# Optimization experiments

Measured on AMD Instinct MI355X. Metric: run time of the kernel, lower is better.

The kernel has to match this reference:

```python
import jax, jax.numpy as jnp
import numpy as np

EPS = 1e-5
ALPHA = 0.7
N_HEADS = 20
N_KV_HEADS = 5
HEAD_DIM = 128


def bitlinear(x, w):
    # absmean ternary quantization per output row: w_t = sign(w)*(|w| > alpha*absmean)
    absw = jnp.abs(w)
    absmean = jnp.mean(absw, axis=1, keepdims=True)            # [out, 1]
    tern = jnp.sign(w) * (absw > ALPHA * absmean).astype(w.dtype)
    # (X @ pos^T - X @ neg^T) * scale == (X @ tern^T) * scale
    return jnp.einsum('...i,oi->...o', x, tern) * absmean[:, 0]


def rmsnorm(x, g):
    var = jnp.mean(jnp.square(x), axis=-1, keepdims=True)
    return x * jax.lax.rsqrt(var + EPS) * g


def rotate_half(x):
    x1, x2 = jnp.split(x, 2, axis=-1)
    return jnp.concatenate([-x2, x1], axis=-1)


def setup_inputs() -> dict:
    key = jax.random.key(0)
    ks = jax.random.split(key, 12)
    h, inter = 2560, 6912
    b, s = 1, 2048
    wscale = 1.0 / np.sqrt(h)
    return {
        'x': jax.random.normal(ks[0], (b, s, h), jnp.float32),
        'cos': jax.random.uniform(ks[1], (1, 1, s, HEAD_DIM), jnp.float32),
        'sin': jax.random.uniform(ks[2], (1, 1, s, HEAD_DIM), jnp.float32),
        'q_w': jax.random.normal(ks[3], (h, h), jnp.float32) * wscale,
        'k_w': jax.random.normal(ks[4], (N_KV_HEADS * HEAD_DIM, h), jnp.float32) * wscale,
        'v_w': jax.random.normal(ks[5], (N_KV_HEADS * HEAD_DIM, h), jnp.float32) * wscale,
        'o_w': jax.random.normal(ks[6], (h, h), jnp.float32) * wscale,
        'gate_w': jax.random.normal(ks[7], (inter, h), jnp.float32) * wscale,
        'up_w': jax.random.normal(ks[8], (inter, h), jnp.float32) * wscale,
        'down_w': jax.random.normal(ks[9], (h, inter), jnp.float32) / np.sqrt(inter),
        'ln1_w': jnp.ones((h,), jnp.float32),
        'ln2_w': jnp.ones((h,), jnp.float32),
    }


def reference(x, cos, sin, q_w, k_w, v_w, o_w, gate_w, up_w, down_w, ln1_w, ln2_w):
    b, s, hdim = x.shape
    residual = x
    h = rmsnorm(x, ln1_w)

    q = bitlinear(h, q_w).reshape(b, s, N_HEADS, HEAD_DIM).transpose(0, 2, 1, 3)
    k = bitlinear(h, k_w).reshape(b, s, N_KV_HEADS, HEAD_DIM).transpose(0, 2, 1, 3)
    v = bitlinear(h, v_w).reshape(b, s, N_KV_HEADS, HEAD_DIM).transpose(0, 2, 1, 3)

    # RoPE
    q = q * cos + rotate_half(q) * sin
    k = k * cos + rotate_half(k) * sin

    # GQA: repeat_interleave kv heads
    n_rep = N_HEADS // N_KV_HEADS
    k = jnp.repeat(k, n_rep, axis=1)
    v = jnp.repeat(v, n_rep, axis=1)

    scale = 1.0 / np.sqrt(HEAD_DIM)
    attn = jnp.einsum('bhqd,bhkd->bhqk', q, k) * scale
    attn = jax.nn.softmax(attn, axis=-1)
    o = jnp.einsum('bhqk,bhkd->bhqd', attn, v)
    o = o.transpose(0, 2, 1, 3).reshape(b, s, hdim)

    x = residual + bitlinear(o, o_w)

    residual = x
    h = rmsnorm(x, ln2_w)
    gate = jnp.square(jax.nn.relu(bitlinear(h, gate_w)))  # relu^2
    x = residual + bitlinear(gate * bitlinear(h, up_w), down_w)
    return x
```

## Files before the change

kernel.cpp:

```cpp
#include <hip/hip_runtime.h>
#include <hip/hip_bf16.h>

typedef unsigned short u16;
typedef short bf16x8 __attribute__((ext_vector_type(8)));
typedef float f32x4 __attribute__((ext_vector_type(4)));
typedef float f32x16 __attribute__((ext_vector_type(16)));
typedef float f4 __attribute__((ext_vector_type(4)));
typedef unsigned short u16x4 __attribute__((ext_vector_type(4)));

__device__ __forceinline__ u16 f2b(float f) {
    union { __hip_bfloat16 h; u16 u; } cv;
    cv.h = __float2bfloat16(f);
    return cv.u;
}
__device__ __forceinline__ float b2f(u16 u) {
    union { u16 u; __hip_bfloat16 h; } cv;
    cv.u = u;
    return __bfloat162float(cv.h);
}

__device__ __forceinline__ void g2l16(const void* g, void* l) {
    __builtin_amdgcn_global_load_lds(
        (const __attribute__((address_space(1))) unsigned int*)g,
        (__attribute__((address_space(3))) unsigned int*)l, 16, 0, 0);
}

template <int NV4, int NS>
__global__ __launch_bounds__(256) void quant_kernel(const float* __restrict__ W,
                                                    u16* __restrict__ T,
                                                    float* __restrict__ scales, int K) {
    const int row = blockIdx.x, tid = threadIdx.x;
    const float* wr = W + (size_t)row * K;
    f4 v[NV4];
    float vs[NS];
    float s = 0.f;
#pragma unroll
    for (int j = 0; j < NV4; ++j) {
        v[j] = ((const f4*)wr)[tid + j * 256];
#pragma unroll
        for (int e = 0; e < 4; ++e) s += fabsf(v[j][e]);
    }
#pragma unroll
    for (int j = 0; j < NS; ++j) { vs[j] = wr[NV4 * 1024 + j * 256 + tid]; s += fabsf(vs[j]); }
#pragma unroll
    for (int d = 1; d < 64; d <<= 1) s += __shfl_xor(s, d);
    __shared__ float red[4];
    if ((tid & 63) == 0) red[tid >> 6] = s;
    __syncthreads();
    const float absmean = (red[0] + red[1] + red[2] + red[3]) / (float)K;
    const float thr = 0.7f * absmean;
    u16* tr = T + (size_t)row * K;
#pragma unroll
    for (int j = 0; j < NV4; ++j) {
        u16x4 o;
#pragma unroll
        for (int e = 0; e < 4; ++e) {
            const float w = v[j][e];
            o[e] = (fabsf(w) > thr) ? ((w > 0.f) ? (u16)0x3F80 : (u16)0xBF80) : (u16)0;
        }
        ((u16x4*)tr)[tid + j * 256] = o;
    }
#pragma unroll
    for (int j = 0; j < NS; ++j) {
        const float w = vs[j];
        tr[NV4 * 1024 + j * 256 + tid] = (fabsf(w) > thr) ? ((w > 0.f) ? (u16)0x3F80 : (u16)0xBF80) : (u16)0;
    }
    if (tid == 0) scales[row] = absmean;
}

__global__ __launch_bounds__(256) void rmsnorm_kernel(const float* __restrict__ x,
                                                      const float* __restrict__ g,
                                                      u16* __restrict__ o) {
    const int row = blockIdx.x, tid = threadIdx.x;
    const float* xr = x + (size_t)row * 2560;
    f4 v[2];
    float vs[2];
    float s = 0.f;
#pragma unroll
    for (int j = 0; j < 2; ++j) {
        v[j] = ((const f4*)xr)[tid + j * 256];
#pragma unroll
        for (int e = 0; e < 4; ++e) s += v[j][e] * v[j][e];
    }
#pragma unroll
    for (int j = 0; j < 2; ++j) { vs[j] = xr[2048 + j * 256 + tid]; s += vs[j] * vs[j]; }
#pragma unroll
    for (int d = 1; d < 64; d <<= 1) s += __shfl_xor(s, d);
    __shared__ float red[4];
    if ((tid & 63) == 0) red[tid >> 6] = s;
    __syncthreads();
    const float total = red[0] + red[1] + red[2] + red[3];
    const float rs = rsqrtf(total * (1.f / 2560.f) + 1e-5f);
    u16* orow = o + (size_t)row * 2560;
#pragma unroll
    for (int j = 0; j < 2; ++j) {
        const f4 gv = ((const f4*)g)[tid + j * 256];
        u16x4 ov;
#pragma unroll
        for (int e = 0; e < 4; ++e) ov[e] = f2b(v[j][e] * rs * gv[e]);
        ((u16x4*)orow)[tid + j * 256] = ov;
    }
#pragma unroll
    for (int j = 0; j < 2; ++j)
        orow[2048 + j * 256 + tid] = f2b(vs[j] * rs * g[2048 + j * 256 + tid]);
}

template <int MODE>
__global__ __launch_bounds__(512, 4) void gemm_bt(const u16* __restrict__ A,
                                                  const u16* __restrict__ B,
                                                  const float* __restrict__ scale,
                                                  const float* res,
                                                  void* __restrict__ outp,
                                                  int M, int N, int K) {
    __shared__ __align__(16) u16 sA[128 * 64];
    __shared__ __align__(16) u16 sB[128 * 64];
    const int tid = threadIdx.x;
    const int wave = tid >> 6, lane = tid & 63;
    const int l31 = lane & 31, half = lane >> 5;
    const int m0 = blockIdx.x * 128, n0 = blockIdx.y * 128;
    const int wm = wave >> 2, wn = wave & 3;

    f32x16 acc[2] = {};

    const int r0 = wave * 8 + (lane >> 3);
    const int gcc = (lane & 7) ^ (lane >> 3);
    const size_t aoff = (size_t)(m0 + r0) * K + gcc * 8;
    const size_t boff = (size_t)(n0 + r0) * K + gcc * 8;
    char* ldsA = (char*)sA + wave * 1024;
    char* ldsB = (char*)sB + wave * 1024;
    const int swz = l31 & 7;
    const int arow0 = (wm * 64 + l31) * 64;
    const int arow1 = (wm * 64 + 32 + l31) * 64;
    const int brow = (wn * 32 + l31) * 64;

    for (int kt = 0; kt < K; kt += 64) {
        g2l16(A + aoff + kt, ldsA);
        g2l16(A + aoff + (size_t)64 * K + kt, ldsA + 8192);
        g2l16(B + boff + kt, ldsB);
        g2l16(B + boff + (size_t)64 * K + kt, ldsB + 8192);
        __syncthreads();
#pragma unroll
        for (int ks = 0; ks < 4; ++ks) {
            const int pc = ((ks * 2 + half) ^ swz) * 8;
            const bf16x8 bfr = *(const bf16x8*)&sB[brow + pc];
            const bf16x8 a0 = *(const bf16x8*)&sA[arow0 + pc];
            const bf16x8 a1 = *(const bf16x8*)&sA[arow1 + pc];
            acc[0] = __builtin_amdgcn_mfma_f32_32x32x16_bf16(a0, bfr, acc[0], 0, 0, 0);
            acc[1] = __builtin_amdgcn_mfma_f32_32x32x16_bf16(a1, bfr, acc[1], 0, 0, 0);
        }
        __syncthreads();
    }

    const int c = n0 + wn * 32 + l31;
    const float sc = scale[c];
#pragma unroll
    for (int mt = 0; mt < 2; ++mt) {
        const int rb = m0 + wm * 64 + mt * 32 + 4 * half;
#pragma unroll
        for (int r = 0; r < 16; ++r) {
            const int row = rb + (r & 3) + 8 * (r >> 2);
            const float vv = acc[mt][r] * sc;
            const size_t idx = (size_t)row * N + c;
            if (MODE == 0)      ((u16*)outp)[idx] = f2b(vv);
            else if (MODE == 1) ((float*)outp)[idx] = res[idx] + vv;
            else {
                const float gg = fmaxf(b2f(((const u16*)res)[idx]), 0.f);
                ((u16*)outp)[idx] = f2b(gg * gg * vv);
            }
        }
    }
}

__global__ __launch_bounds__(256) void rope_kernel(u16* __restrict__ buf, int stride,
                                                   const float* __restrict__ cs,
                                                   const float* __restrict__ sn, int nh) {
    const int idx = blockIdx.x * 256 + threadIdx.x;
    const int d = idx & 63;
    const int h = (idx >> 6) % nh;
    const int s = idx / (64 * nh);
    const size_t base = (size_t)s * stride + h * 128;
    const float a = b2f(buf[base + d]), b = b2f(buf[base + d + 64]);
    const float c1 = cs[s * 128 + d], s1 = sn[s * 128 + d];
    const float c2 = cs[s * 128 + d + 64], s2 = sn[s * 128 + d + 64];
    buf[base + d] = f2b(a * c1 - b * s1);
    buf[base + d + 64] = f2b(b * c2 + a * s2);
}

__global__ __launch_bounds__(256) void transpose_v_kernel(const u16* __restrict__ V, int stride,
                                                          u16* __restrict__ VT) {
    __shared__ u16 t[128 * 66];
    const int tid = threadIdx.x;
    const int h = blockIdx.y, s0 = blockIdx.x * 64;
#pragma unroll
    for (int i = 0; i < 32; ++i) {
        const int idx = tid + i * 256;
        const int r = idx >> 7, c = idx & 127;
        t[c * 66 + r] = V[(size_t)(s0 + r) * stride + h * 128 + c];
    }
    __syncthreads();
#pragma unroll
    for (int i = 0; i < 32; ++i) {
        const int idx = tid + i * 256;
        const int d = idx >> 6, s = idx & 63;
        VT[((size_t)h * 128 + d) * 2048 + s0 + s] = t[d * 66 + s];
    }
}

__global__ __launch_bounds__(256, 3) void flash_kernel(const u16* __restrict__ Q, int qs,
                                                       const u16* __restrict__ Kb,
                                                       const u16* __restrict__ VT,
                                                       u16* __restrict__ O) {
    __shared__ __align__(16) u16 sQ[64 * 128];
    __shared__ __align__(16) u16 sK[2][32 * 128];
    __shared__ __align__(16) u16 sV[2][128 * 32];
    const int tid = threadIdx.x, wave = tid >> 6, lane = tid & 63;
    const int lane15 = lane & 15, quad = lane >> 4;
    const int head = blockIdx.y, q0 = blockIdx.x * 64, kvh = head >> 2;
    const int sw = lane15 & 7;

    const int rk = wave * 4 + (lane >> 4);
    const int gk = (lane & 15) ^ (rk & 7);
    const u16* kbase = Kb + (size_t)rk * qs + kvh * 128 + gk * 8;
    const int rv = wave * 16 + (lane >> 2);
    const int gv = (lane & 3) ^ ((lane >> 3) & 3);
    const u16* vbase = VT + ((size_t)kvh * 128 + rv) * 2048 + gv * 8;

    auto stage = [&](int k0, int b) {
        char* dK = (char*)(&sK[b][0]) + wave * 1024;
        char* dV = (char*)(&sV[b][0]) + wave * 1024;
#pragma unroll
        for (int s = 0; s < 2; ++s) {
            g2l16(kbase + ((size_t)k0 + s * 16) * qs, dK + s * 4096);
            g2l16(vbase + (size_t)s * 64 * 2048 + k0, dV + s * 4096);
        }
    };

    {
        const int rq = wave * 4 + (lane >> 4);
        const int gq = (lane & 15) ^ (rq & 7);
        const u16* src = Q + (size_t)(q0 + rq) * qs + head * 128 + gq * 8;
        char* dst = (char*)sQ + wave * 1024;
#pragma unroll
        for (int s = 0; s < 4; ++s)
            g2l16(src + (size_t)s * 16 * qs, dst + s * 4096);
        stage(0, 0);
    }
    __syncthreads();
    bf16x8 qf[4];
#pragma unroll
    for (int kc = 0; kc < 4; ++kc)
        qf[kc] = *(const bf16x8*)&sQ[(wave * 16 + lane15) * 128 + ((kc * 4 + quad) ^ sw) * 8];

    float m_i[4], lp[4];
    f32x4 o_acc[8] = {};
#pragma unroll
    for (int r = 0; r < 4; ++r) { m_i[r] = -1e30f; lp[r] = 0.f; }

    const float sl2e = 0.088388347648318447f * 1.4426950408889634f;
    const float THR = 8.0f;
    u16* sP = sQ;

    for (int t = 0; t < 64; ++t) {
        const int buf = t & 1;
        if (t < 63) stage((t + 1) * 32, buf ^ 1);
        const u16* sKb = &sK[buf][0];
        const u16* sVb = &sV[buf][0];

        f32x4 sacc[2] = {};
        __builtin_amdgcn_s_setprio(1);
#pragma unroll
        for (int nf = 0; nf < 2; ++nf)
#pragma unroll
            for (int kc = 0; kc < 4; ++kc) {
                const bf16x8 kf = *(const bf16x8*)&sKb[(nf * 16 + lane15) * 128 + ((kc * 4 + quad) ^ sw) * 8];
                sacc[nf] = __builtin_amdgcn_mfma_f32_16x16x32_bf16(qf[kc], kf, sacc[nf], 0, 0, 0);
            }
        __builtin_amdgcn_s_setprio(0);

        float mx[4];
#pragma unroll
        for (int r = 0; r < 4; ++r) {
            float v0 = sacc[0][r] * sl2e, v1 = sacc[1][r] * sl2e;
            sacc[0][r] = v0; sacc[1][r] = v1;
            float m0 = fmaxf(v0, v1);
#pragma unroll
            for (int d = 1; d < 16; d <<= 1) m0 = fmaxf(m0, __shfl_xor(m0, d));
            mx[r] = m0;
        }
        const int upd = (mx[0] > m_i[0] + THR) | (mx[1] > m_i[1] + THR) |
                        (mx[2] > m_i[2] + THR) | (mx[3] > m_i[3] + THR);
        if (__any(upd)) {
#pragma unroll
            for (int r = 0; r < 4; ++r) {
                const float mnew = fmaxf(m_i[r], mx[r]);
                const float alpha = exp2f(m_i[r] - mnew);
                m_i[r] = mnew;
                lp[r] *= alpha;
#pragma unroll
                for (int nf = 0; nf < 8; ++nf) o_acc[nf][r] *= alpha;
            }
        }
#pragma unroll
        for (int r = 0; r < 4; ++r) {
            const float m = m_i[r];
            const float p0 = exp2f(sacc[0][r] - m), p1 = exp2f(sacc[1][r] - m);
            sacc[0][r] = p0; sacc[1][r] = p1;
            lp[r] += p0 + p1;
        }

#pragma unroll
        for (int nf = 0; nf < 2; ++nf) {
            const int pcol = nf * 16 + lane15;
#pragma unroll
            for (int r = 0; r < 4; ++r)
                sP[(wave * 16 + quad * 4 + r) * 40 + pcol] = f2b(sacc[nf][r]);
        }

        const bf16x8 pf = *(const bf16x8*)&sP[(wave * 16 + lane15) * 40 + quad * 8];
        __builtin_amdgcn_s_setprio(1);
#pragma unroll
        for (int nf = 0; nf < 8; ++nf) {
            const bf16x8 vf = *(const bf16x8*)&sVb[(nf * 16 + lane15) * 32 +
                                                   ((quad ^ ((lane15 >> 1) & 3))) * 8];
            o_acc[nf] = __builtin_amdgcn_mfma_f32_16x16x32_bf16(pf, vf, o_acc[nf], 0, 0, 0);
        }
        __builtin_amdgcn_s_setprio(0);
        __syncthreads();
    }

#pragma unroll
    for (int r = 0; r < 4; ++r) {
        float lt = lp[r];
#pragma unroll
        for (int d = 1; d < 16; d <<= 1) lt += __shfl_xor(lt, d);
        const float inv = 1.f / lt;
        const int row = q0 + wave * 16 + quad * 4 + r;
        u16* orow = O + (size_t)row * 2560 + head * 128;
#pragma unroll
        for (int nf = 0; nf < 8; ++nf)
            orow[nf * 16 + lane15] = f2b(o_acc[nf][r] * inv);
    }
}

extern "C" void kernel_launch(void* const* d_in, const int* in_sizes, int n_in,
                              void* d_out, int out_size, void* d_ws, size_t ws_size,
                              hipStream_t stream) {
    (void)in_sizes; (void)n_in; (void)out_size; (void)ws_size;
    const float* x      = (const float*)d_in[0];
    const float* cosb   = (const float*)d_in[1];
    const float* sinb   = (const float*)d_in[2];
    const float* q_w    = (const float*)d_in[3];
    const float* k_w    = (const float*)d_in[4];
    const float* v_w    = (const float*)d_in[5];
    const float* o_w    = (const float*)d_in[6];
    const float* gate_w = (const float*)d_in[7];
    const float* up_w   = (const float*)d_in[8];
    const float* down_w = (const float*)d_in[9];
    const float* ln1    = (const float*)d_in[10];
    const float* ln2    = (const float*)d_in[11];

    char* w = (char*)d_ws;
    size_t off = 0;
    auto nxt = [&](size_t sz) { char* p = w + off; off += sz; return p; };
    u16*   TQ = (u16*)nxt(13107200);
    u16*   TK = (u16*)nxt(3276800);
    u16*   TV = (u16*)nxt(3276800);
    u16*   TO = (u16*)nxt(13107200);
    u16*   TB = (u16*)nxt(35389440);
    float* SC = (float*)nxt(91136);
    u16*   H  = (u16*)nxt(10485760);
    u16*   QKV = (u16*)nxt(15728640);
    u16*   VT = (u16*)nxt(2621440);
    float* XM = (float*)nxt(20971520);
    u16*   G  = (u16*)nxt(28311552);

    quant_kernel<2, 2><<<2560, 256, 0, stream>>>(q_w, TQ, SC + 0, 2560);
    quant_kernel<2, 2><<<640, 256, 0, stream>>>(k_w, TK, SC + 2560, 2560);
    quant_kernel<2, 2><<<640, 256, 0, stream>>>(v_w, TV, SC + 3200, 2560);
    quant_kernel<2, 2><<<2560, 256, 0, stream>>>(o_w, TO, SC + 3840, 2560);
    rmsnorm_kernel<<<2048, 256, 0, stream>>>(x, ln1, H);
    gemm_bt<0><<<dim3(16, 30), 512, 0, stream>>>(H, TQ, SC + 0, nullptr, QKV, 2048, 3840, 2560);
    rope_kernel<<<10240, 256, 0, stream>>>(QKV, 3840, cosb, sinb, 20);
    rope_kernel<<<2560, 256, 0, stream>>>(QKV + 2560, 3840, cosb, sinb, 5);
    transpose_v_kernel<<<dim3(32, 5), 256, 0, stream>>>(QKV + 3200, 3840, VT);
    flash_kernel<<<dim3(32, 20), 256, 0, stream>>>(QKV, 3840, QKV + 2560, VT, H);
    gemm_bt<1><<<dim3(16, 20), 512, 0, stream>>>(H, TO, SC + 3840, x, XM, 2048, 2560, 2560);

    rmsnorm_kernel<<<2048, 256, 0, stream>>>(XM, ln2, H);
    quant_kernel<2, 2><<<6912, 256, 0, stream>>>(gate_w, TB, SC + 6400, 2560);
    gemm_bt<0><<<dim3(16, 54), 512, 0, stream>>>(H, TB, SC + 6400, nullptr, G, 2048, 6912, 2560);
    quant_kernel<2, 2><<<6912, 256, 0, stream>>>(up_w, TB, SC + 13312, 2560);
    gemm_bt<2><<<dim3(16, 54), 512, 0, stream>>>(H, TB, SC + 13312, (const float*)G, G, 2048, 6912, 2560);
    quant_kernel<6, 3><<<2560, 256, 0, stream>>>(down_w, TB, SC + 20224, 6912);
    gemm_bt<1><<<dim3(16, 20), 512, 0, stream>>>(G, TB, SC + 20224, XM, (float*)d_out, 2048, 2560, 6912);
}
```

Before: 861.7 us.

## Double-buffer GEMM LDS tiles and remap workgroups across XCDs for L2 locality

The GEMM kernel gets two LDS buffers per operand and prefetches the next K tile while the MFMAs run on the current one, so the global-to-LDS load no longer stalls behind a barrier each iteration. Both the GEMM and flash-attention kernels remap the linear workgroup id so that consecutive tiles land on the same XCD (stride of 8), aiming to improve L2 reuse of shared A/B or K/V rows. Double buffering doubles GEMM LDS use to 64 KB per block, which may lower occupancy under the 4-blocks launch bound. The remap assumes the grid size divides by 8 (and is hardcoded to 32x20 for flash).

```diff
diff --git a/kernel.cpp b/kernel.cpp
--- a/kernel.cpp
+++ b/kernel.cpp
@@ -112,12 +112,16 @@
                                                   const float* res,
                                                   void* __restrict__ outp,
                                                   int M, int N, int K) {
-    __shared__ __align__(16) u16 sA[128 * 64];
-    __shared__ __align__(16) u16 sB[128 * 64];
+    __shared__ __align__(16) u16 sA[2][128 * 64];
+    __shared__ __align__(16) u16 sB[2][128 * 64];
     const int tid = threadIdx.x;
     const int wave = tid >> 6, lane = tid & 63;
     const int l31 = lane & 31, half = lane >> 5;
-    const int m0 = blockIdx.x * 128, n0 = blockIdx.y * 128;
+
+    const int nwg = gridDim.x * gridDim.y;
+    int lin = blockIdx.y * gridDim.x + blockIdx.x;
+    lin = (lin & 7) * (nwg >> 3) + (lin >> 3);
+    const int m0 = (lin % gridDim.x) * 128, n0 = (lin / gridDim.x) * 128;
     const int wm = wave >> 2, wn = wave & 3;
 
     f32x16 acc[2] = {};
@@ -126,25 +130,34 @@
     const int gcc = (lane & 7) ^ (lane >> 3);
     const size_t aoff = (size_t)(m0 + r0) * K + gcc * 8;
     const size_t boff = (size_t)(n0 + r0) * K + gcc * 8;
-    char* ldsA = (char*)sA + wave * 1024;
-    char* ldsB = (char*)sB + wave * 1024;
     const int swz = l31 & 7;
     const int arow0 = (wm * 64 + l31) * 64;
     const int arow1 = (wm * 64 + 32 + l31) * 64;
     const int brow = (wn * 32 + l31) * 64;
 
-    for (int kt = 0; kt < K; kt += 64) {
+    auto stage = [&](int kt, int b) {
+        char* ldsA = (char*)(&sA[b][0]) + wave * 1024;
+        char* ldsB = (char*)(&sB[b][0]) + wave * 1024;
         g2l16(A + aoff + kt, ldsA);
         g2l16(A + aoff + (size_t)64 * K + kt, ldsA + 8192);
         g2l16(B + boff + kt, ldsB);
         g2l16(B + boff + (size_t)64 * K + kt, ldsB + 8192);
-        __syncthreads();
+    };
+
+    stage(0, 0);
+    __syncthreads();
+    const int nk = K >> 6;
+    for (int t = 0; t < nk; ++t) {
+        const int buf = t & 1;
+        if (t + 1 < nk) stage((t + 1) * 64, buf ^ 1);
+        const u16* pA = &sA[buf][0];
+        const u16* pB = &sB[buf][0];
 #pragma unroll
         for (int ks = 0; ks < 4; ++ks) {
             const int pc = ((ks * 2 + half) ^ swz) * 8;
-            const bf16x8 bfr = *(const bf16x8*)&sB[brow + pc];
-            const bf16x8 a0 = *(const bf16x8*)&sA[arow0 + pc];
-            const bf16x8 a1 = *(const bf16x8*)&sA[arow1 + pc];
+            const bf16x8 bfr = *(const bf16x8*)&pB[brow + pc];
+            const bf16x8 a0 = *(const bf16x8*)&pA[arow0 + pc];
+            const bf16x8 a1 = *(const bf16x8*)&pA[arow1 + pc];
             acc[0] = __builtin_amdgcn_mfma_f32_32x32x16_bf16(a0, bfr, acc[0], 0, 0, 0);
             acc[1] = __builtin_amdgcn_mfma_f32_32x32x16_bf16(a1, bfr, acc[1], 0, 0, 0);
         }
@@ -215,7 +228,9 @@
     __shared__ __align__(16) u16 sV[2][128 * 32];
     const int tid = threadIdx.x, wave = tid >> 6, lane = tid & 63;
     const int lane15 = lane & 15, quad = lane >> 4;
-    const int head = blockIdx.y, q0 = blockIdx.x * 64, kvh = head >> 2;
+    int lin = blockIdx.y * 32 + blockIdx.x;
+    lin = (lin & 7) * 80 + (lin >> 3);
+    const int head = lin >> 5, q0 = (lin & 31) * 64, kvh = head >> 2;
     const int sw = lane15 & 7;
 
     const int rk = wave * 4 + (lane >> 4);
```

After: 863.4 us. About the same (+0.2%).

## Add 256x128 GEMM tile variant with 2x2 MFMA per wave and XCD-aware block remap

Applied to the files above, without the earlier changes.

Templates the GEMM on a fragment count so the QKV, gate and up projections use a 256x128 block tile. Each wave now computes a 64x64 sub-tile with 2x2 MFMAs, which cuts LDS reads per MFMA and halves the number of times the weight matrix is re-read from memory. It also remaps linear block ids in strides of eight so that neighbouring tiles land on the same XCD, aiming for better L2 reuse. The cost is more LDS per block, which may limit how many blocks fit on a CU, and fewer blocks overall, which can underfill the GPU for the QKV GEMM (240 blocks).

```diff
diff --git a/kernel.cpp b/kernel.cpp
--- a/kernel.cpp
+++ b/kernel.cpp
@@ -105,67 +105,84 @@
         orow[2048 + j * 256 + tid] = f2b(vs[j] * rs * g[2048 + j * 256 + tid]);
 }
 
-template <int MODE>
+template <int MODE, int NFR>
 __global__ __launch_bounds__(512, 4) void gemm_bt(const u16* __restrict__ A,
                                                   const u16* __restrict__ B,
                                                   const float* __restrict__ scale,
                                                   const float* res,
                                                   void* __restrict__ outp,
                                                   int M, int N, int K) {
-    __shared__ __align__(16) u16 sA[128 * 64];
+    constexpr int TM = 128 * NFR;
+    __shared__ __align__(16) u16 sA[TM * 64];
     __shared__ __align__(16) u16 sB[128 * 64];
     const int tid = threadIdx.x;
     const int wave = tid >> 6, lane = tid & 63;
     const int l31 = lane & 31, half = lane >> 5;
-    const int m0 = blockIdx.x * 128, n0 = blockIdx.y * 128;
-    const int wm = wave >> 2, wn = wave & 3;
-
-    f32x16 acc[2] = {};
+
+    const int nwg = gridDim.x * gridDim.y;
+    int lin = blockIdx.y * gridDim.x + blockIdx.x;
+    lin = (lin & 7) * (nwg >> 3) + (lin >> 3);
+    const int m0 = (lin % gridDim.x) * TM, n0 = (lin / gridDim.x) * 128;
+    const int wm = (NFR == 2) ? (wave >> 1) : (wave >> 2);
+    const int wn = (NFR == 2) ? (wave & 1) : (wave & 3);
+
+    f32x16 acc[2][NFR] = {};
 
     const int r0 = wave * 8 + (lane >> 3);
     const int gcc = (lane & 7) ^ (lane >> 3);
     const size_t aoff = (size_t)(m0 + r0) * K + gcc * 8;
     const size_t boff = (size_t)(n0 + r0) * K + gcc * 8;
+    const int swz = l31 & 7;
     char* ldsA = (char*)sA + wave * 1024;
     char* ldsB = (char*)sB + wave * 1024;
-    const int swz = l31 & 7;
-    const int arow0 = (wm * 64 + l31) * 64;
-    const int arow1 = (wm * 64 + 32 + l31) * 64;
-    const int brow = (wn * 32 + l31) * 64;
 
     for (int kt = 0; kt < K; kt += 64) {
-        g2l16(A + aoff + kt, ldsA);
-        g2l16(A + aoff + (size_t)64 * K + kt, ldsA + 8192);
-        g2l16(B + boff + kt, ldsB);
-        g2l16(B + boff + (size_t)64 * K + kt, ldsB + 8192);
+#pragma unroll
+        for (int s = 0; s < TM / 64; ++s)
+            g2l16(A + aoff + (size_t)(s * 64) * K + kt, ldsA + s * 8192);
+#pragma unroll
+        for (int s = 0; s < 2; ++s)
+            g2l16(B + boff + (size_t)(s * 64) * K + kt, ldsB + s * 8192);
         __syncthreads();
 #pragma unroll
         for (int ks = 0; ks < 4; ++ks) {
             const int pc = ((ks * 2 + half) ^ swz) * 8;
-            const bf16x8 bfr = *(const bf16x8*)&sB[brow + pc];
-            const bf16x8 a0 = *(const bf16x8*)&sA[arow0 + pc];
-            const bf16x8 a1 = *(const bf16x8*)&sA[arow1 + pc];
-            acc[0] = __builtin_amdgcn_mfma_f32_32x32x16_bf16(a0, bfr, acc[0], 0, 0, 0);
-            acc[1] = __builtin_amdgcn_mfma_f32_32x32x16_bf16(a1, bfr, acc[1], 0, 0, 0);
+            bf16x8 af[2], bfr[NFR];
+            af[0] = *(const bf16x8*)&sA[(wm * 64 + l31) * 64 + pc];
+            af[1] = *(const bf16x8*)&sA[(wm * 64 + 32 + l31) * 64 + pc];
+            if (NFR == 1) {
+                bfr[0] = *(const bf16x8*)&sB[(wn * 32 + l31) * 64 + pc];
+            } else {
+                bfr[0] = *(const bf16x8*)&sB[(wn * 64 + l31) * 64 + pc];
+                bfr[1] = *(const bf16x8*)&sB[(wn * 64 + 32 + l31) * 64 + pc];
+            }
+#pragma unroll
+            for (int mt = 0; mt < 2; ++mt)
+#pragma unroll
+                for (int nt = 0; nt < NFR; ++nt)
+                    acc[mt][nt] = __builtin_amdgcn_mfma_f32_32x32x16_bf16(af[mt], bfr[nt], acc[mt][nt], 0, 0, 0);
         }
         __syncthreads();
     }
 
-    const int c = n0 + wn * 32 + l31;
-    const float sc = scale[c];
-#pragma unroll
-    for (int mt = 0; mt < 2; ++mt) {
-        const int rb = m0 + wm * 64 + mt * 32 + 4 * half;
-#pragma unroll
-        for (int r = 0; r < 16; ++r) {
-            const int row = rb + (r & 3) + 8 * (r >> 2);
-            const float vv = acc[mt][r] * sc;
-            const size_t idx = (size_t)row * N + c;
-            if (MODE == 0)      ((u16*)outp)[idx] = f2b(vv);
-            else if (MODE == 1) ((float*)outp)[idx] = res[idx] + vv;
-            else {
-                const float gg = fmaxf(b2f(((const u16*)res)[idx]), 0.f);
-                ((u16*)outp)[idx] = f2b(gg * gg * vv);
+#pragma unroll
+    for (int nt = 0; nt < NFR; ++nt) {
+        const int c = n0 + ((NFR == 1) ? wn * 32 : wn * 64 + nt * 32) + l31;
+        const float sc = scale[c];
+#pragma unroll
+        for (int mt = 0; mt < 2; ++mt) {
+            const int rb = m0 + wm * 64 + mt * 32 + 4 * half;
+#pragma unroll
+            for (int r = 0; r < 16; ++r) {
+                const int row = rb + (r & 3) + 8 * (r >> 2);
+                const float vv = acc[mt][nt][r] * sc;
+                const size_t idx = (size_t)row * N + c;
+                if (MODE == 0)      ((u16*)outp)[idx] = f2b(vv);
+                else if (MODE == 1) ((float*)outp)[idx] = res[idx] + vv;
+                else {
+                    const float gg = fmaxf(b2f(((const u16*)res)[idx]), 0.f);
+                    ((u16*)outp)[idx] = f2b(gg * gg * vv);
+                }
             }
         }
     }
@@ -379,18 +396,18 @@
     quant_kernel<2, 2><<<640, 256, 0, stream>>>(v_w, TV, SC + 3200, 2560);
     quant_kernel<2, 2><<<2560, 256, 0, stream>>>(o_w, TO, SC + 3840, 2560);
     rmsnorm_kernel<<<2048, 256, 0, stream>>>(x, ln1, H);
-    gemm_bt<0><<<dim3(16, 30), 512, 0, stream>>>(H, TQ, SC + 0, nullptr, QKV, 2048, 3840, 2560);
+    gemm_bt<0, 2><<<dim3(8, 30), 512, 0, stream>>>(H, TQ, SC + 0, nullptr, QKV, 2048, 3840, 2560);
     rope_kernel<<<10240, 256, 0, stream>>>(QKV, 3840, cosb, sinb, 20);
     rope_kernel<<<2560, 256, 0, stream>>>(QKV + 2560, 3840, cosb, sinb, 5);
     transpose_v_kernel<<<dim3(32, 5), 256, 0, stream>>>(QKV + 3200, 3840, VT);
     flash_kernel<<<dim3(32, 20), 256, 0, stream>>>(QKV, 3840, QKV + 2560, VT, H);
-    gemm_bt<1><<<dim3(16, 20), 512, 0, stream>>>(H, TO, SC + 3840, x, XM, 2048, 2560, 2560);
+    gemm_bt<1, 1><<<dim3(16, 20), 512, 0, stream>>>(H, TO, SC + 3840, x, XM, 2048, 2560, 2560);
 
     rmsnorm_kernel<<<2048, 256, 0, stream>>>(XM, ln2, H);
     quant_kernel<2, 2><<<6912, 256, 0, stream>>>(gate_w, TB, SC + 6400, 2560);
-    gemm_bt<0><<<dim3(16, 54), 512, 0, stream>>>(H, TB, SC + 6400, nullptr, G, 2048, 6912, 2560);
+    gemm_bt<0, 2><<<dim3(8, 54), 512, 0, stream>>>(H, TB, SC + 6400, nullptr, G, 2048, 6912, 2560);
     quant_kernel<2, 2><<<6912, 256, 0, stream>>>(up_w, TB, SC + 13312, 2560);
-    gemm_bt<2><<<dim3(16, 54), 512, 0, stream>>>(H, TB, SC + 13312, (const float*)G, G, 2048, 6912, 2560);
+    gemm_bt<2, 2><<<dim3(8, 54), 512, 0, stream>>>(H, TB, SC + 13312, (const float*)G, G, 2048, 6912, 2560);
     quant_kernel<6, 3><<<2560, 256, 0, stream>>>(down_w, TB, SC + 20224, 6912);
-    gemm_bt<1><<<dim3(16, 20), 512, 0, stream>>>(G, TB, SC + 20224, XM, (float*)d_out, 2048, 2560, 6912);
-}
+    gemm_bt<1, 1><<<dim3(16, 20), 512, 0, stream>>>(G, TB, SC + 20224, XM, (float*)d_out, 2048, 2560, 6912);
+}
```

Result: no change. 862.3 us (+0.1%).
